# Kernel tuning notes

Measured on AMD Instinct MI355X. Metric: run time of the kernel, lower is better.

Reference implementation:

```python
import jax, jax.numpy as jnp
import numpy as np

B, L, E, H, V, T, NL = 32, 512, 512, 1024, 32000, 64, 2


def setup_inputs() -> dict:
    key = jax.random.key(0)
    ks = jax.random.split(key, 24)
    u = lambda k, s, a=0.05: jax.random.uniform(k, s, jnp.float32, -a, a)
    return {
        "enc_output": jax.random.normal(ks[0], (B, L, H), jnp.float32),
        "trg": jax.random.randint(ks[1], (B, T), 0, V, dtype=jnp.int64),
        "emb": u(ks[2], (V, E), 0.1),
        "W_att_enc": u(ks[3], (H, H)), "b_att_enc": jnp.zeros((H,), jnp.float32),
        "W_att_dec": u(ks[4], (H, H)), "b_att_dec": jnp.zeros((H,), jnp.float32),
        "v_att": u(ks[5], (H,)),
        "W_in": u(ks[6], (E, E + H)), "b_in": jnp.zeros((E,), jnp.float32),
        "W_ih0": u(ks[7], (4 * H, E)), "W_hh0": u(ks[8], (4 * H, H)),
        "b_ih0": jnp.zeros((4 * H,), jnp.float32), "b_hh0": jnp.zeros((4 * H,), jnp.float32),
        "W_ih1": u(ks[9], (4 * H, H)), "W_hh1": u(ks[10], (4 * H, H)),
        "b_ih1": jnp.zeros((4 * H,), jnp.float32), "b_hh1": jnp.zeros((4 * H,), jnp.float32),
        "W_fc": u(ks[11], (V, H), 0.1), "b_fc": jnp.zeros((V,), jnp.float32),
        "is_train": 0, "is_test": 1, "max_len": T, "sos_idx": 1,
    }


def _lstm_cell(x, h, c, W_ih, W_hh, b_ih, b_hh):
    g = x @ W_ih.T + b_ih + h @ W_hh.T + b_hh  # [B, 4H]
    i, f, gg, o = jnp.split(g, 4, axis=-1)     # torch gate order i,f,g,o
    c2 = jax.nn.sigmoid(f) * c + jax.nn.sigmoid(i) * jnp.tanh(gg)
    h2 = jax.nn.sigmoid(o) * jnp.tanh(c2)
    return h2, c2


def reference(enc_output, trg, emb, W_att_enc, b_att_enc, W_att_dec, b_att_dec,
              v_att, W_in, b_in, W_ih0, W_hh0, b_ih0, b_hh0, W_ih1, W_hh1,
              b_ih1, b_hh1, W_fc, b_fc, is_train, is_test, max_len, sos_idx):
    b = trg.shape[0]
    # precompute encoder projection for additive attention: [B, L, H]
    enc_proj = jnp.einsum('blh,ah->bla', enc_output, W_att_enc) + b_att_enc

    def step(carry, _):
        h, c, token = carry                    # h, c: [NL, B, H]
        emb_t = emb[token]                     # [B, E]
        q = h[-1] @ W_att_dec.T + b_att_dec    # [B, H]
        energy = jnp.tanh(enc_proj + q[:, None, :])
        alpha = jax.nn.softmax(energy @ v_att, axis=-1)        # [B, L]
        ctx = jnp.einsum('bl,blh->bh', alpha, enc_output)      # [B, H]
        x = jnp.concatenate([emb_t, ctx], axis=-1) @ W_in.T + b_in  # [B, E]
        h0, c0 = _lstm_cell(x, h[0], c[0], W_ih0, W_hh0, b_ih0, b_hh0)
        h1, c1 = _lstm_cell(h0, h[1], c[1], W_ih1, W_hh1, b_ih1, b_hh1)
        pred = h1 @ W_fc.T + b_fc              # [B, V]
        tok = jnp.argmax(pred, axis=1).astype(jnp.int32)
        return (jnp.stack([h0, h1]), jnp.stack([c0, c1]), tok), (pred, tok)

    h0 = jnp.zeros((NL, b, H), jnp.float32)
    init = (h0, h0, trg[:, 0].astype(jnp.int32))
    _, (preds, toks) = jax.lax.scan(step, init, None, length=max_len - 1)
    outputs = jnp.concatenate([jnp.zeros((1, b, V), preds.dtype), preds], 0)
    outputs = outputs.transpose(1, 0, 2)       # [B, max_len, V]
    _pred = jnp.concatenate(
        [jnp.full((b, 1), sos_idx, jnp.int32), toks.T], axis=1).astype(jnp.float32)
    return outputs, _pred
```

## Files before the change

kernel.cpp:

```cpp
#include <hip/hip_runtime.h>
#include <math.h>

#define BB 32
#define LL 512
#define EE 512
#define HH 1024
#define VV 32000
#define TT 64
#define G4 4096
#define NPRED 33024

__device__ __forceinline__ float fast_tanh(float x){
  float ax = fabsf(x);
  float e = __expf(ax + ax);
  float r = 1.0f - 2.0f/(e + 1.0f);
  return copysignf(r, x);
}

__global__ void k_init(float* __restrict__ outp, float* __restrict__ a0t,
                       float* __restrict__ a1t, float* __restrict__ c0,
                       float* __restrict__ c1, float* __restrict__ q,
                       const float* __restrict__ bad, int* __restrict__ token,
                       const int* __restrict__ trg, const int* __restrict__ sosp,
                       float* __restrict__ predout){
  int idx = blockIdx.x*256 + threadIdx.x;
  if (idx < 1024000){ int b = idx / VV; int v = idx % VV;
    outp[(size_t)b*TT*VV + v] = 0.f; return; }
  idx -= 1024000;
  if (idx < 49152){ a0t[idx]=0.f; return; } idx -= 49152;
  if (idx < 65536){ a1t[idx]=0.f; return; } idx -= 65536;
  if (idx < 32768){ c0[idx]=0.f; return; } idx -= 32768;
  if (idx < 32768){ c1[idx]=0.f; return; } idx -= 32768;
  if (idx < 32768){ q[idx] = bad[idx & (HH-1)]; return; } idx -= 32768;
  if (idx < 32){ token[idx] = trg[idx*TT]; return; } idx -= 32;
  if (idx < 32){ predout[idx*TT] = (float)(*sosp); return; }
}

__global__ void k_transpose(const float* __restrict__ src, int ss,
                            float* __restrict__ dst, int ds, int R, int C){
  __shared__ float tile[32][33];
  int c0 = blockIdx.x*32, r0 = blockIdx.y*32;
  int tx = threadIdx.x, ty = threadIdx.y;
  #pragma unroll
  for (int i=0;i<32;i+=8)
    tile[ty+i][tx] = src[(size_t)(r0+ty+i)*ss + c0+tx];
  __syncthreads();
  #pragma unroll
  for (int i=0;i<32;i+=8)
    dst[(size_t)(c0+ty+i)*ds + r0+tx] = tile[tx][ty+i];
}

__global__ __launch_bounds__(256) void k_pregemm(const float* __restrict__ AT,
    const float* __restrict__ WT, const float* __restrict__ bias,
    float* __restrict__ Cout, int N, int Kdim){
  int mt = blockIdx.x, ntg = blockIdx.y;
  int w = threadIdx.x >> 6, lane = threadIdx.x & 63;
  int m0 = mt*128 + lane;
  int nbase = ntg*128 + w*32;
  float acc0[32], acc1[32];
  #pragma unroll
  for (int j=0;j<32;j++){ acc0[j]=0.f; acc1[j]=0.f; }
  const float* ap = AT + m0;
  const float* wp = WT + nbase;
  for (int k=0;k<Kdim;k++){
    float a0 = ap[(size_t)k*16384];
    float a1 = ap[(size_t)k*16384 + 64];
    const float4* w4 = (const float4*)(wp + (size_t)k*N);
    #pragma unroll
    for (int j4=0;j4<8;j4++){
      float4 wv = w4[j4];
      acc0[j4*4+0] = fmaf(a0, wv.x, acc0[j4*4+0]);
      acc0[j4*4+1] = fmaf(a0, wv.y, acc0[j4*4+1]);
      acc0[j4*4+2] = fmaf(a0, wv.z, acc0[j4*4+2]);
      acc0[j4*4+3] = fmaf(a0, wv.w, acc0[j4*4+3]);
      acc1[j4*4+0] = fmaf(a1, wv.x, acc1[j4*4+0]);
      acc1[j4*4+1] = fmaf(a1, wv.y, acc1[j4*4+1]);
      acc1[j4*4+2] = fmaf(a1, wv.z, acc1[j4*4+2]);
      acc1[j4*4+3] = fmaf(a1, wv.w, acc1[j4*4+3]);
    }
  }
  __shared__ float tile[64][133];
  #pragma unroll
  for (int j=0;j<32;j++){
    float bv = bias ? bias[nbase+j] : 0.f;
    tile[lane][w*32+j] = acc0[j] + bv;
  }
  __syncthreads();
  #pragma unroll
  for (int i=0;i<32;i++){
    int flat = i*256 + threadIdx.x;
    int mm = flat >> 7, nn = flat & 127;
    Cout[(size_t)(mt*128+mm)*N + ntg*128 + nn] = tile[mm][nn];
  }
  __syncthreads();
  #pragma unroll
  for (int j=0;j<32;j++){
    float bv = bias ? bias[nbase+j] : 0.f;
    tile[lane][w*32+j] = acc1[j] + bv;
  }
  __syncthreads();
  #pragma unroll
  for (int i=0;i<32;i++){
    int flat = i*256 + threadIdx.x;
    int mm = flat >> 7, nn = flat & 127;
    Cout[(size_t)(mt*128+64+mm)*N + ntg*128 + nn] = tile[mm][nn];
  }
}

__global__ __launch_bounds__(256) void k_scorepred(const float* __restrict__ ep,
    const float* __restrict__ partP, const float* __restrict__ bad,
    const float* __restrict__ vatt, float* __restrict__ scores,
    const float* __restrict__ b_fc, float* __restrict__ outp,
    float* __restrict__ argv, int* __restrict__ argi, int t){
  int vb = blockIdx.x;
  int w = threadIdx.x >> 6, lane = threadIdx.x & 63;
  if (vb < 1024){
    int b = vb & 31, lt = vb >> 5;
    __shared__ float qs[HH], vs[HH];
    for (int i=threadIdx.x; i<HH; i+=256){
      float qv = bad[i];
      if (t > 1){
        qv += partP[(size_t)b*NPRED + VV + i]
            + partP[(size_t)(32+b)*NPRED + VV + i]
            + partP[(size_t)(64+b)*NPRED + VV + i]
            + partP[(size_t)(96+b)*NPRED + VV + i];
      }
      qs[i] = qv;
      vs[i] = vatt[i];
    }
    __syncthreads();
    #pragma unroll
    for (int i=0;i<4;i++){
      int l = lt*16 + w*4 + i;
      const float4* row = (const float4*)(ep + ((size_t)(b*LL + l))*HH);
      float acc = 0.f;
      #pragma unroll
      for (int c=0;c<4;c++){
        float4 xv = row[c*64 + lane];
        float4 qv = ((const float4*)qs)[c*64 + lane];
        float4 vv = ((const float4*)vs)[c*64 + lane];
        acc += fast_tanh(xv.x+qv.x)*vv.x;
        acc += fast_tanh(xv.y+qv.y)*vv.y;
        acc += fast_tanh(xv.z+qv.z)*vv.z;
        acc += fast_tanh(xv.w+qv.w)*vv.w;
      }
      #pragma unroll
      for (int d=32; d>0; d>>=1) acc += __shfl_down(acc, d);
      if (lane==0) scores[b*LL + l] = acc;
    }
  } else {
    if (t <= 1) return;
    int pb = vb - 1024;
    int n = pb*256 + threadIdx.x;
    int tm1 = t - 1;
    float bias = b_fc[n];
    const float* p0 = partP + n;
    const float* p1 = partP + (size_t)32*NPRED + n;
    const float* p2 = partP + (size_t)64*NPRED + n;
    const float* p3 = partP + (size_t)96*NPRED + n;
    for (int b=0;b<32;b++){
      float v = p0[(size_t)b*NPRED] + p1[(size_t)b*NPRED]
              + p2[(size_t)b*NPRED] + p3[(size_t)b*NPRED] + bias;
      outp[(size_t)(b*TT + tm1)*VV + n] = v;
      float bv = v; int bi = n;
      #pragma unroll
      for (int d=32; d>0; d>>=1){
        float ov = __shfl_down(bv, d); int oi = __shfl_down(bi, d);
        if (ov > bv || (ov==bv && oi < bi)){ bv=ov; bi=oi; }
      }
      if (lane==0){
        argv[(pb*4 + w)*32 + b] = bv;
        argi[(pb*4 + w)*32 + b] = bi;
      }
    }
  }
}

__global__ __launch_bounds__(512) void k_attnx(const float* __restrict__ scores,
    const float* __restrict__ encW2, const float* __restrict__ emb,
    const int* __restrict__ token, const float* __restrict__ W1T,
    const float* __restrict__ b_in, float* __restrict__ A0T,
    const float* __restrict__ argv, const int* __restrict__ argi,
    float* __restrict__ predout, int t){
  int b = blockIdx.x, et = blockIdx.y;
  int tx = threadIdx.x;
  int w = tx >> 6, lane = tx & 63;
  __shared__ float alpha[LL];
  __shared__ float embs[EE];
  __shared__ float redm[8], reds[8];
  __shared__ float comb[8][64];
  __shared__ int tokS;
  if (t > 1){
    if (w==0){
      float bv = -INFINITY; int bi = 0x7fffffff;
      for (int j=lane; j<500; j+=64){
        float v = argv[j*32 + b]; int ix = argi[j*32 + b];
        if (v > bv || (v==bv && ix < bi)){ bv=v; bi=ix; }
      }
      #pragma unroll
      for (int d=32; d>0; d>>=1){
        float ov = __shfl_down(bv, d); int oi = __shfl_down(bi, d);
        if (ov > bv || (ov==bv && oi < bi)){ bv=ov; bi=oi; }
      }
      if (lane==0){
        tokS = bi;
        if (et==0) predout[b*TT + (t-1)] = (float)bi;
      }
    }
  } else if (tx==0) tokS = token[b];
  float s = scores[b*LL + tx];
  float mx = s;
  #pragma unroll
  for (int d=32; d>0; d>>=1) mx = fmaxf(mx, __shfl_down(mx, d));
  if (lane==0) redm[w] = mx;
  __syncthreads();
  mx = redm[0];
  #pragma unroll
  for (int i=1;i<8;i++) mx = fmaxf(mx, redm[i]);
  float e0 = __expf(s - mx);
  float sm = e0;
  #pragma unroll
  for (int d=32; d>0; d>>=1) sm += __shfl_down(sm, d);
  if (lane==0) reds[w] = sm;
  __syncthreads();
  sm = reds[0]+reds[1]+reds[2]+reds[3]+reds[4]+reds[5]+reds[6]+reds[7];
  alpha[tx] = e0 / sm;
  int tok = tokS;
  embs[tx] = emb[(size_t)tok*EE + tx];
  __syncthreads();
  int e = et*64 + lane;
  float acc = 0.f;
  const float* cw = encW2 + (size_t)b*LL*EE + (size_t)w*64*EE + e;
  #pragma unroll 8
  for (int l=0;l<64;l++) acc = fmaf(alpha[w*64+l], cw[(size_t)l*EE], acc);
  const float* wp = W1T + (size_t)w*64*EE + e;
  #pragma unroll 8
  for (int j=0;j<64;j++) acc = fmaf(embs[w*64+j], wp[(size_t)j*EE], acc);
  comb[w][lane] = acc;
  __syncthreads();
  if (w==0){
    float r = comb[0][lane]+comb[1][lane]+comb[2][lane]+comb[3][lane]
            + comb[4][lane]+comb[5][lane]+comb[6][lane]+comb[7][lane] + b_in[e];
    A0T[e*32 + b] = r;
  }
}

__device__ __forceinline__ void fma_step(float (&acc)[8][4], const float4 wv,
                                         const float4 a0, const float4 a1){
  acc[0][0]=fmaf(a0.x,wv.x,acc[0][0]); acc[0][1]=fmaf(a0.x,wv.y,acc[0][1]);
  acc[0][2]=fmaf(a0.x,wv.z,acc[0][2]); acc[0][3]=fmaf(a0.x,wv.w,acc[0][3]);
  acc[1][0]=fmaf(a0.y,wv.x,acc[1][0]); acc[1][1]=fmaf(a0.y,wv.y,acc[1][1]);
  acc[1][2]=fmaf(a0.y,wv.z,acc[1][2]); acc[1][3]=fmaf(a0.y,wv.w,acc[1][3]);
  acc[2][0]=fmaf(a0.z,wv.x,acc[2][0]); acc[2][1]=fmaf(a0.z,wv.y,acc[2][1]);
  acc[2][2]=fmaf(a0.z,wv.z,acc[2][2]); acc[2][3]=fmaf(a0.z,wv.w,acc[2][3]);
  acc[3][0]=fmaf(a0.w,wv.x,acc[3][0]); acc[3][1]=fmaf(a0.w,wv.y,acc[3][1]);
  acc[3][2]=fmaf(a0.w,wv.z,acc[3][2]); acc[3][3]=fmaf(a0.w,wv.w,acc[3][3]);
  acc[4][0]=fmaf(a1.x,wv.x,acc[4][0]); acc[4][1]=fmaf(a1.x,wv.y,acc[4][1]);
  acc[4][2]=fmaf(a1.x,wv.z,acc[4][2]); acc[4][3]=fmaf(a1.x,wv.w,acc[4][3]);
  acc[5][0]=fmaf(a1.y,wv.x,acc[5][0]); acc[5][1]=fmaf(a1.y,wv.y,acc[5][1]);
  acc[5][2]=fmaf(a1.y,wv.z,acc[5][2]); acc[5][3]=fmaf(a1.y,wv.w,acc[5][3]);
  acc[6][0]=fmaf(a1.z,wv.x,acc[6][0]); acc[6][1]=fmaf(a1.z,wv.y,acc[6][1]);
  acc[6][2]=fmaf(a1.z,wv.z,acc[6][2]); acc[6][3]=fmaf(a1.z,wv.w,acc[6][3]);
  acc[7][0]=fmaf(a1.w,wv.x,acc[7][0]); acc[7][1]=fmaf(a1.w,wv.y,acc[7][1]);
  acc[7][2]=fmaf(a1.w,wv.z,acc[7][2]); acc[7][3]=fmaf(a1.w,wv.w,acc[7][3]);
}

template<int KSLICE>
__global__ __launch_bounds__(256) void k_gemm2(const float* __restrict__ AT,
    const float* __restrict__ WT, float* __restrict__ partial, int N){
  __shared__ __align__(16) float As[KSLICE*32];
  int nt = blockIdx.x, ks = blockIdx.y;
  int w = threadIdx.x >> 6, lane = threadIdx.x & 63;
  int k0 = ks*KSLICE;
  const float4* asrc = (const float4*)(AT + (size_t)k0*32);
  for (int i=threadIdx.x; i<KSLICE*8; i+=256)
    ((float4*)As)[i] = asrc[i];
  __syncthreads();
  int n0 = nt*256 + lane*4;
  int b0 = w*8;
  float acc[8][4];
  #pragma unroll
  for (int i=0;i<8;i++)
    #pragma unroll
    for (int j=0;j<4;j++) acc[i][j]=0.f;
  const float* wp = WT + (size_t)k0*N + n0;
  const float* ap = As + b0;
  float4 w0 = *(const float4*)(wp);
  float4 w1 = *(const float4*)(wp + (size_t)N);
  float4 w2 = *(const float4*)(wp + (size_t)2*N);
  float4 w3 = *(const float4*)(wp + (size_t)3*N);
  wp += (size_t)4*N;
#define GSTEP(WREG) { float4 a0 = *(const float4*)(ap); \
                      float4 a1 = *(const float4*)(ap+4); ap += 32; \
                      fma_step(acc, WREG, a0, a1); }
  for (int k=0; k<KSLICE-4; k+=4){
    float4 p0 = *(const float4*)(wp);
    float4 p1 = *(const float4*)(wp + (size_t)N);
    float4 p2 = *(const float4*)(wp + (size_t)2*N);
    float4 p3 = *(const float4*)(wp + (size_t)3*N);
    wp += (size_t)4*N;
    GSTEP(w0); GSTEP(w1); GSTEP(w2); GSTEP(w3);
    w0 = p0; w1 = p1; w2 = p2; w3 = p3;
  }
  GSTEP(w0); GSTEP(w1); GSTEP(w2); GSTEP(w3);
#undef GSTEP
  float* pp = partial + ((size_t)ks*32 + b0)*N + n0;
  #pragma unroll
  for (int bi=0;bi<8;bi++)
    *(float4*)(pp + (size_t)bi*N) =
      make_float4(acc[bi][0],acc[bi][1],acc[bi][2],acc[bi][3]);
}

template<int KSLICE>
__global__ __launch_bounds__(256) void k_gemm2w8(const float* __restrict__ AT,
    const float* __restrict__ WT, float* __restrict__ partial, int N){
  __shared__ __align__(16) float As[KSLICE*32];
  int nt = blockIdx.x, ks = blockIdx.y;
  int w = threadIdx.x >> 6, lane = threadIdx.x & 63;
  int k0 = ks*KSLICE;
  const float4* asrc = (const float4*)(AT + (size_t)k0*32);
  for (int i=threadIdx.x; i<KSLICE*8; i+=256)
    ((float4*)As)[i] = asrc[i];
  __syncthreads();
  int n0 = nt*256 + lane*4;
  int b0 = w*8;
  float acc[8][4];
  #pragma unroll
  for (int i=0;i<8;i++)
    #pragma unroll
    for (int j=0;j<4;j++) acc[i][j]=0.f;
  const float* wp = WT + (size_t)k0*N + n0;
  const float* ap = As + b0;
  float4 w0 = *(const float4*)(wp);
  float4 w1 = *(const float4*)(wp + (size_t)N);
  float4 w2 = *(const float4*)(wp + (size_t)2*N);
  float4 w3 = *(const float4*)(wp + (size_t)3*N);
  float4 w4 = *(const float4*)(wp + (size_t)4*N);
  float4 w5 = *(const float4*)(wp + (size_t)5*N);
  float4 w6 = *(const float4*)(wp + (size_t)6*N);
  float4 w7 = *(const float4*)(wp + (size_t)7*N);
  wp += (size_t)8*N;
#define GSTEP(WREG) { float4 a0 = *(const float4*)(ap); \
                      float4 a1 = *(const float4*)(ap+4); ap += 32; \
                      fma_step(acc, WREG, a0, a1); }
  for (int k=0; k<KSLICE-8; k+=8){
    float4 p0 = *(const float4*)(wp);
    float4 p1 = *(const float4*)(wp + (size_t)N);
    float4 p2 = *(const float4*)(wp + (size_t)2*N);
    float4 p3 = *(const float4*)(wp + (size_t)3*N);
    float4 p4 = *(const float4*)(wp + (size_t)4*N);
    float4 p5 = *(const float4*)(wp + (size_t)5*N);
    float4 p6 = *(const float4*)(wp + (size_t)6*N);
    float4 p7 = *(const float4*)(wp + (size_t)7*N);
    wp += (size_t)8*N;
    GSTEP(w0); GSTEP(w1); GSTEP(w2); GSTEP(w3);
    GSTEP(w4); GSTEP(w5); GSTEP(w6); GSTEP(w7);
    w0=p0; w1=p1; w2=p2; w3=p3; w4=p4; w5=p5; w6=p6; w7=p7;
  }
  GSTEP(w0); GSTEP(w1); GSTEP(w2); GSTEP(w3);
  GSTEP(w4); GSTEP(w5); GSTEP(w6); GSTEP(w7);
#undef GSTEP
  float* pp = partial + ((size_t)ks*32 + b0)*N + n0;
  #pragma unroll
  for (int bi=0;bi<8;bi++)
    *(float4*)(pp + (size_t)bi*N) =
      make_float4(acc[bi][0],acc[bi][1],acc[bi][2],acc[bi][3]);
}

__global__ __launch_bounds__(128) void k_cell(const float* __restrict__ partial,
    const float* __restrict__ b_ih, const float* __restrict__ b_hh,
    float* __restrict__ c, float* __restrict__ hdst1, float* __restrict__ hdst2){
  int idx = blockIdx.x*128 + threadIdx.x;
  int b = idx >> 10, h = idx & 1023;
  const float* pb = partial + (size_t)b*G4;
  float gi = b_ih[h]      + b_hh[h];
  float gf = b_ih[1024+h] + b_hh[1024+h];
  float gg = b_ih[2048+h] + b_hh[2048+h];
  float go = b_ih[3072+h] + b_hh[3072+h];
  #pragma unroll 8
  for (int ks=0; ks<32; ks++){
    const float* pp = pb + (size_t)ks*32*G4;
    gi += pp[h]; gf += pp[1024+h]; gg += pp[2048+h]; go += pp[3072+h];
  }
  float cv = c[idx];
  float si = 1.f/(1.f+expf(-gi));
  float sf = 1.f/(1.f+expf(-gf));
  float so = 1.f/(1.f+expf(-go));
  float tg = tanhf(gg);
  float c2 = sf*cv + si*tg;
  float h2 = so*tanhf(c2);
  c[idx] = c2;
  hdst1[h*32 + b] = h2;
  if (hdst2) hdst2[h*32 + b] = h2;
}

__global__ __launch_bounds__(256) void k_predsum(const float* __restrict__ partP,
    const float* __restrict__ b_fc, float* __restrict__ outp,
    float* __restrict__ argv, int* __restrict__ argi, int t){
  int n = blockIdx.x*256 + threadIdx.x;
  int w = threadIdx.x >> 6, lane = threadIdx.x & 63;
  float bias = b_fc[n];
  const float* p0 = partP + n;
  const float* p1 = partP + (size_t)32*NPRED + n;
  const float* p2 = partP + (size_t)64*NPRED + n;
  const float* p3 = partP + (size_t)96*NPRED + n;
  for (int b=0;b<32;b++){
    float v = p0[(size_t)b*NPRED] + p1[(size_t)b*NPRED]
            + p2[(size_t)b*NPRED] + p3[(size_t)b*NPRED] + bias;
    outp[(size_t)(b*TT + t)*VV + n] = v;
    float bv = v; int bi = n;
    #pragma unroll
    for (int d=32; d>0; d>>=1){
      float ov = __shfl_down(bv, d); int oi = __shfl_down(bi, d);
      if (ov > bv || (ov==bv && oi < bi)){ bv=ov; bi=oi; }
    }
    if (lane==0){
      argv[(blockIdx.x*4 + w)*32 + b] = bv;
      argi[(blockIdx.x*4 + w)*32 + b] = bi;
    }
  }
}

__global__ void k_argfinal(const float* __restrict__ argv,
                           const int* __restrict__ argi,
                           float* __restrict__ predout){
  int b = threadIdx.x >> 3, j = threadIdx.x & 7;
  float bv = -INFINITY; int bi = 0x7fffffff;
  for (int p=j; p<500; p+=8){
    float v = argv[p*32+b]; int ix = argi[p*32+b];
    if (v>bv || (v==bv && ix<bi)){ bv=v; bi=ix; }
  }
  #pragma unroll
  for (int d=4; d>0; d>>=1){
    float ov = __shfl_down(bv, d); int oi = __shfl_down(bi, d);
    if (ov>bv || (ov==bv && oi<bi)){ bv=ov; bi=oi; }
  }
  if (j==0) predout[b*TT + 63] = (float)bi;
}

extern "C" void kernel_launch(void* const* d_in, const int* in_sizes, int n_in,
                              void* d_out, int out_size, void* d_ws, size_t ws_size,
                              hipStream_t stream){
  const float* enc_output=(const float*)d_in[0];
  const int*   trg       =(const int*)d_in[1];
  const float* emb       =(const float*)d_in[2];
  const float* W_att_enc =(const float*)d_in[3];
  const float* b_att_enc =(const float*)d_in[4];
  const float* W_att_dec =(const float*)d_in[5];
  const float* b_att_dec =(const float*)d_in[6];
  const float* v_att     =(const float*)d_in[7];
  const float* W_in      =(const float*)d_in[8];
  const float* b_in      =(const float*)d_in[9];
  const float* W_ih0     =(const float*)d_in[10];
  const float* W_hh0     =(const float*)d_in[11];
  const float* b_ih0     =(const float*)d_in[12];
  const float* b_hh0     =(const float*)d_in[13];
  const float* W_ih1     =(const float*)d_in[14];
  const float* W_hh1     =(const float*)d_in[15];
  const float* b_ih1     =(const float*)d_in[16];
  const float* b_hh1     =(const float*)d_in[17];
  const float* W_fc      =(const float*)d_in[18];
  const float* b_fc      =(const float*)d_in[19];
  const int*   sosp      =(const int*)d_in[23];

  float* out = (float*)d_out;
  float* predout = out + (size_t)BB*TT*VV;
  float* ws = (float*)d_ws;

  float* WcatPT = ws;
  float* Wcat0T = ws + 33816576;
  float* Wcat1T = ws + 40108032;
  float* W1T    = ws + 48496640;
  float* WinCtxT= ws + 48758784;
  float* WattET = ws + 49283072;
  float* encT   = ws + 50331648;
  float* partP  = encT;
  float* ep     = ws + 67108864;
  float* encW2  = ws + 83886080;
  float* partLS = ws + 92274688;
  float* A0T    = ws + 96468992;
  float* A1T    = ws + 96518144;
  float* c0     = ws + 96583680;
  float* c1     = ws + 96616448;
  float* q      = ws + 96649216;
  float* scores = ws + 96681984;
  float* argv   = ws + 96698368;
  int*   argi   = (int*)(ws + 96714368);
  int*   token  = (int*)(ws + 96730368);

  k_init<<<dim3(4833), dim3(256), 0, stream>>>(out, A0T, A1T, c0, c1, q,
      b_att_dec, token, trg, sosp, predout);

  auto TR=[&](const float* src,int ss,float* dst,int ds,int R,int C){
    k_transpose<<<dim3(C/32, R/32), dim3(32,8), 0, stream>>>(src, ss, dst, ds, R, C);
  };
  TR(W_fc, 1024, WcatPT, NPRED, VV, 1024);
  TR(W_att_dec, 1024, WcatPT + VV, NPRED, 1024, 1024);
  TR(W_ih0, 512, Wcat0T, G4, G4, 512);
  TR(W_hh0, 1024, Wcat0T + (size_t)512*G4, G4, G4, 1024);
  TR(W_ih1, 1024, Wcat1T, G4, G4, 1024);
  TR(W_hh1, 1024, Wcat1T + (size_t)1024*G4, G4, G4, 1024);
  TR(W_in, 1536, W1T, 512, 512, 512);
  TR(W_in + 512, 1536, WinCtxT, 512, 512, 1024);
  TR(W_att_enc, 1024, WattET, 1024, 1024, 1024);
  TR(enc_output, 1024, encT, 16384, 16384, 1024);

  k_pregemm<<<dim3(128,8), dim3(256), 0, stream>>>(encT, WattET, b_att_enc, ep, 1024, 1024);
  k_pregemm<<<dim3(128,4), dim3(256), 0, stream>>>(encT, WinCtxT, nullptr, encW2, 512, 1024);

  for (int t=1; t<TT; t++){
    k_scorepred<<<dim3(1149), dim3(256), 0, stream>>>(ep, partP, b_att_dec, v_att,
        scores, b_fc, out, argv, argi, t);
    k_attnx<<<dim3(32,8), dim3(512), 0, stream>>>(scores, encW2, emb, token,
        W1T, b_in, A0T, argv, argi, predout, t);
    k_gemm2<48><<<dim3(16,32), dim3(256), 0, stream>>>(A0T, Wcat0T, partLS, G4);
    k_cell<<<dim3(256), dim3(128), 0, stream>>>(partLS, b_ih0, b_hh0, c0,
        A0T + (size_t)512*32, A1T);
    k_gemm2<64><<<dim3(16,32), dim3(256), 0, stream>>>(A1T, Wcat1T, partLS, G4);
    k_cell<<<dim3(256), dim3(128), 0, stream>>>(partLS, b_ih1, b_hh1, c1,
        A1T + (size_t)1024*32, nullptr);
    k_gemm2w8<256><<<dim3(129,4), dim3(256), 0, stream>>>(A1T + (size_t)1024*32,
        WcatPT, partP, NPRED);
  }
  k_predsum<<<dim3(125), dim3(256), 0, stream>>>(partP, b_fc, out, argv, argi, 63);
  k_argfinal<<<dim3(1), dim3(256), 0, stream>>>(argv, argi, predout);
}
```

Measured before the change: 11.67 ms.

## Pack recurrent weight matrices into contiguous per-block tiles for skinny GEMMs

Adds a transpose-and-pack kernel that stores each weight matrix as contiguous [kslice][ntile][KSLICE][256] tiles, so each GEMM block streams one contiguous chunk instead of rows strided by N. The two LSTM GEMMs and the output-projection GEMM now share a single kernel that uses the 8-deep register prefetch, where the LSTM GEMMs previously prefetched only 4 rows ahead. This is meant to improve DRAM and cache-line locality and prefetch depth on the bandwidth-bound per-step weight reads. It adds index arithmetic to the one-time packing and more register pressure in the LSTM GEMMs.

```diff
diff --git a/kernel.cpp b/kernel.cpp
--- a/kernel.cpp
+++ b/kernel.cpp
@@ -48,6 +48,25 @@
   #pragma unroll
   for (int i=0;i<32;i+=8)
     dst[(size_t)(c0+ty+i)*ds + r0+tx] = tile[tx][ty+i];
+}
+
+__global__ void k_transpack(const float* __restrict__ src, int ss,
+                            float* __restrict__ dst, int KS, int NT,
+                            int kOff, int nOff){
+  __shared__ float tile[32][33];
+  int c0 = blockIdx.x*32, r0 = blockIdx.y*32;
+  int tx = threadIdx.x, ty = threadIdx.y;
+  #pragma unroll
+  for (int i=0;i<32;i+=8)
+    tile[ty+i][tx] = src[(size_t)(r0+ty+i)*ss + c0+tx];
+  __syncthreads();
+  #pragma unroll
+  for (int i=0;i<32;i+=8){
+    int k = kOff + c0 + ty + i;
+    int n = nOff + r0 + tx;
+    int ks = k / KS, kk = k - ks*KS;
+    dst[((size_t)(ks*NT + (n>>8))*KS + kk)*256 + (n&255)] = tile[tx][ty+i];
+  }
 }
 
 __global__ __launch_bounds__(256) void k_pregemm(const float* __restrict__ AT,
@@ -266,8 +285,8 @@
 }
 
 template<int KSLICE>
-__global__ __launch_bounds__(256) void k_gemm2(const float* __restrict__ AT,
-    const float* __restrict__ WT, float* __restrict__ partial, int N){
+__global__ __launch_bounds__(256) void k_gemm3(const float* __restrict__ AT,
+    const float* __restrict__ WP, float* __restrict__ partial, int N, int NT){
   __shared__ __align__(16) float As[KSLICE*32];
   int nt = blockIdx.x, ks = blockIdx.y;
   int w = threadIdx.x >> 6, lane = threadIdx.x & 63;
@@ -283,76 +302,30 @@
   for (int i=0;i<8;i++)
     #pragma unroll
     for (int j=0;j<4;j++) acc[i][j]=0.f;
-  const float* wp = WT + (size_t)k0*N + n0;
+  const float* wp = WP + (size_t)(ks*NT + nt)*KSLICE*256 + lane*4;
   const float* ap = As + b0;
   float4 w0 = *(const float4*)(wp);
-  float4 w1 = *(const float4*)(wp + (size_t)N);
-  float4 w2 = *(const float4*)(wp + (size_t)2*N);
-  float4 w3 = *(const float4*)(wp + (size_t)3*N);
-  wp += (size_t)4*N;
-#define GSTEP(WREG) { float4 a0 = *(const float4*)(ap); \
-                      float4 a1 = *(const float4*)(ap+4); ap += 32; \
-                      fma_step(acc, WREG, a0, a1); }
-  for (int k=0; k<KSLICE-4; k+=4){
-    float4 p0 = *(const float4*)(wp);
-    float4 p1 = *(const float4*)(wp + (size_t)N);
-    float4 p2 = *(const float4*)(wp + (size_t)2*N);
-    float4 p3 = *(const float4*)(wp + (size_t)3*N);
-    wp += (size_t)4*N;
-    GSTEP(w0); GSTEP(w1); GSTEP(w2); GSTEP(w3);
-    w0 = p0; w1 = p1; w2 = p2; w3 = p3;
-  }
-  GSTEP(w0); GSTEP(w1); GSTEP(w2); GSTEP(w3);
-#undef GSTEP
-  float* pp = partial + ((size_t)ks*32 + b0)*N + n0;
-  #pragma unroll
-  for (int bi=0;bi<8;bi++)
-    *(float4*)(pp + (size_t)bi*N) =
-      make_float4(acc[bi][0],acc[bi][1],acc[bi][2],acc[bi][3]);
-}
-
-template<int KSLICE>
-__global__ __launch_bounds__(256) void k_gemm2w8(const float* __restrict__ AT,
-    const float* __restrict__ WT, float* __restrict__ partial, int N){
-  __shared__ __align__(16) float As[KSLICE*32];
-  int nt = blockIdx.x, ks = blockIdx.y;
-  int w = threadIdx.x >> 6, lane = threadIdx.x & 63;
-  int k0 = ks*KSLICE;
-  const float4* asrc = (const float4*)(AT + (size_t)k0*32);
-  for (int i=threadIdx.x; i<KSLICE*8; i+=256)
-    ((float4*)As)[i] = asrc[i];
-  __syncthreads();
-  int n0 = nt*256 + lane*4;
-  int b0 = w*8;
-  float acc[8][4];
-  #pragma unroll
-  for (int i=0;i<8;i++)
-    #pragma unroll
-    for (int j=0;j<4;j++) acc[i][j]=0.f;
-  const float* wp = WT + (size_t)k0*N + n0;
-  const float* ap = As + b0;
-  float4 w0 = *(const float4*)(wp);
-  float4 w1 = *(const float4*)(wp + (size_t)N);
-  float4 w2 = *(const float4*)(wp + (size_t)2*N);
-  float4 w3 = *(const float4*)(wp + (size_t)3*N);
-  float4 w4 = *(const float4*)(wp + (size_t)4*N);
-  float4 w5 = *(const float4*)(wp + (size_t)5*N);
-  float4 w6 = *(const float4*)(wp + (size_t)6*N);
-  float4 w7 = *(const float4*)(wp + (size_t)7*N);
-  wp += (size_t)8*N;
+  float4 w1 = *(const float4*)(wp + 256);
+  float4 w2 = *(const float4*)(wp + 512);
+  float4 w3 = *(const float4*)(wp + 768);
+  float4 w4 = *(const float4*)(wp + 1024);
+  float4 w5 = *(const float4*)(wp + 1280);
+  float4 w6 = *(const float4*)(wp + 1536);
+  float4 w7 = *(const float4*)(wp + 1792);
+  wp += 2048;
 #define GSTEP(WREG) { float4 a0 = *(const float4*)(ap); \
                       float4 a1 = *(const float4*)(ap+4); ap += 32; \
                       fma_step(acc, WREG, a0, a1); }
   for (int k=0; k<KSLICE-8; k+=8){
     float4 p0 = *(const float4*)(wp);
-    float4 p1 = *(const float4*)(wp + (size_t)N);
-    float4 p2 = *(const float4*)(wp + (size_t)2*N);
-    float4 p3 = *(const float4*)(wp + (size_t)3*N);
-    float4 p4 = *(const float4*)(wp + (size_t)4*N);
-    float4 p5 = *(const float4*)(wp + (size_t)5*N);
-    float4 p6 = *(const float4*)(wp + (size_t)6*N);
-    float4 p7 = *(const float4*)(wp + (size_t)7*N);
-    wp += (size_t)8*N;
+    float4 p1 = *(const float4*)(wp + 256);
+    float4 p2 = *(const float4*)(wp + 512);
+    float4 p3 = *(const float4*)(wp + 768);
+    float4 p4 = *(const float4*)(wp + 1024);
+    float4 p5 = *(const float4*)(wp + 1280);
+    float4 p6 = *(const float4*)(wp + 1536);
+    float4 p7 = *(const float4*)(wp + 1792);
+    wp += 2048;
     GSTEP(w0); GSTEP(w1); GSTEP(w2); GSTEP(w3);
     GSTEP(w4); GSTEP(w5); GSTEP(w6); GSTEP(w7);
     w0=p0; w1=p1; w2=p2; w3=p3; w4=p4; w5=p5; w6=p6; w7=p7;
@@ -467,9 +440,9 @@
   float* predout = out + (size_t)BB*TT*VV;
   float* ws = (float*)d_ws;
 
-  float* WcatPT = ws;
-  float* Wcat0T = ws + 33816576;
-  float* Wcat1T = ws + 40108032;
+  float* WPackP = ws;
+  float* WPack0 = ws + 33816576;
+  float* WPack1 = ws + 40108032;
   float* W1T    = ws + 48496640;
   float* WinCtxT= ws + 48758784;
   float* WattET = ws + 49283072;
@@ -494,12 +467,17 @@
   auto TR=[&](const float* src,int ss,float* dst,int ds,int R,int C){
     k_transpose<<<dim3(C/32, R/32), dim3(32,8), 0, stream>>>(src, ss, dst, ds, R, C);
   };
-  TR(W_fc, 1024, WcatPT, NPRED, VV, 1024);
-  TR(W_att_dec, 1024, WcatPT + VV, NPRED, 1024, 1024);
-  TR(W_ih0, 512, Wcat0T, G4, G4, 512);
-  TR(W_hh0, 1024, Wcat0T + (size_t)512*G4, G4, G4, 1024);
-  TR(W_ih1, 1024, Wcat1T, G4, G4, 1024);
-  TR(W_hh1, 1024, Wcat1T + (size_t)1024*G4, G4, G4, 1024);
+  auto TP=[&](const float* src,int ss,float* dst,int KS,int NT,int kOff,int nOff,
+              int R,int C){
+    k_transpack<<<dim3(C/32, R/32), dim3(32,8), 0, stream>>>(src, ss, dst,
+        KS, NT, kOff, nOff);
+  };
+  TP(W_fc,      1024, WPackP, 256, 129, 0,    0,  VV,   1024);
+  TP(W_att_dec, 1024, WPackP, 256, 129, 0,    VV, 1024, 1024);
+  TP(W_ih0,     512,  WPack0, 48,  16,  0,    0,  G4,   512);
+  TP(W_hh0,     1024, WPack0, 48,  16,  512,  0,  G4,   1024);
+  TP(W_ih1,     1024, WPack1, 64,  16,  0,    0,  G4,   1024);
+  TP(W_hh1,     1024, WPack1, 64,  16,  1024, 0,  G4,   1024);
   TR(W_in, 1536, W1T, 512, 512, 512);
   TR(W_in + 512, 1536, WinCtxT, 512, 512, 1024);
   TR(W_att_enc, 1024, WattET, 1024, 1024, 1024);
@@ -513,14 +491,14 @@
         scores, b_fc, out, argv, argi, t);
     k_attnx<<<dim3(32,8), dim3(512), 0, stream>>>(scores, encW2, emb, token,
         W1T, b_in, A0T, argv, argi, predout, t);
-    k_gemm2<48><<<dim3(16,32), dim3(256), 0, stream>>>(A0T, Wcat0T, partLS, G4);
+    k_gemm3<48><<<dim3(16,32), dim3(256), 0, stream>>>(A0T, WPack0, partLS, G4, 16);
     k_cell<<<dim3(256), dim3(128), 0, stream>>>(partLS, b_ih0, b_hh0, c0,
         A0T + (size_t)512*32, A1T);
-    k_gemm2<64><<<dim3(16,32), dim3(256), 0, stream>>>(A1T, Wcat1T, partLS, G4);
+    k_gemm3<64><<<dim3(16,32), dim3(256), 0, stream>>>(A1T, WPack1, partLS, G4, 16);
     k_cell<<<dim3(256), dim3(128), 0, stream>>>(partLS, b_ih1, b_hh1, c1,
         A1T + (size_t)1024*32, nullptr);
-    k_gemm2w8<256><<<dim3(129,4), dim3(256), 0, stream>>>(A1T + (size_t)1024*32,
-        WcatPT, partP, NPRED);
+    k_gemm3<256><<<dim3(129,4), dim3(256), 0, stream>>>(A1T + (size_t)1024*32,
+        WPackP, partP, NPRED, 129);
   }
   k_predsum<<<dim3(125), dim3(256), 0, stream>>>(partP, b_fc, out, argv, argi, 63);
   k_argfinal<<<dim3(1), dim3(256), 0, stream>>>(argv, argi, predout);
```

Result: faster. 11.04 ms (-5.5%).
